# Kernel optimization log

Hardware: AMD Instinct MI355X
Metric: run time of the kernel (lower is better)

## Reference

```python
import jax, jax.numpy as jnp
import numpy as np

N = 1_000_000      # total atoms
B = 1024           # number of molecules (batch segments)
NUM_ELEMENTS = 118
D_EMB = 64
D_HID = 128


def setup_inputs() -> dict:
    key = jax.random.key(0)
    ks = jax.random.split(key, 9)
    positions = jax.random.normal(ks[0], (N, 3), dtype=jnp.float32) * 5.0
    atomic_numbers = jax.random.randint(ks[1], (N,), 0, NUM_ELEMENTS, dtype=jnp.int64)
    batch = jnp.sort(jax.random.randint(ks[2], (N,), 0, B, dtype=jnp.int64))
    # learned parameters (torch Linear is y = x @ W.T + b; we store W as (in, out))
    embed = jax.random.normal(ks[3], (NUM_ELEMENTS, D_EMB), dtype=jnp.float32) * 0.1
    W1 = jax.random.normal(ks[4], (D_EMB, D_HID), dtype=jnp.float32) * (1.0 / np.sqrt(D_EMB))
    b1 = jnp.zeros((D_HID,), dtype=jnp.float32)
    W2 = jax.random.normal(ks[5], (D_HID, D_HID), dtype=jnp.float32) * (1.0 / np.sqrt(D_HID))
    b2 = jnp.zeros((D_HID,), dtype=jnp.float32)
    W3 = jax.random.normal(ks[6], (D_HID, 1), dtype=jnp.float32) * (1.0 / np.sqrt(D_HID))
    b3 = jnp.zeros((1,), dtype=jnp.float32)
    return {
        "positions": positions,
        "embed": embed,
        "W1": W1, "b1": b1,
        "W2": W2, "b2": b2,
        "W3": W3, "b3": b3,
        "atomic_numbers": atomic_numbers,
        "batch": batch,
    }


def reference(positions, embed, W1, b1, W2, b2, W3, b3, atomic_numbers, batch):
    def energy_fn(pos):
        h = embed[atomic_numbers]                       # [N, 64] gather
        pos_feat = jnp.sum(pos, axis=-1, keepdims=True) # [N, 1]
        h = h + 0.0 * pos_feat                          # keeps pos in the graph (grad is zero)
        x = jax.nn.silu(h @ W1 + b1)                    # [N, 128]
        x = jax.nn.silu(x @ W2 + b2)                    # [N, 128]
        per_atom = (x @ W3 + b3)[:, 0]                  # [N]
        # energy.scatter_add_(0, batch, per_atom)
        return jax.ops.segment_sum(per_atom, batch, num_segments=B)  # [B]

    energy = energy_fn(positions)
    # forces = -grad_R sum(V(R)); identically zero here but computed faithfully
    forces = -jax.grad(lambda p: energy_fn(p).sum())(positions)      # [N, 3]
    return (energy, forces)
```

## Files before the change

kernel.cpp:

```cpp
#include <hip/hip_runtime.h>

#define D_EMB   64
#define D_HID   128
#define NUM_EL  118
#define CHUNK   1024
#define NBINS   16

__global__ __launch_bounds__(256)
void mace_etab_kernel(const float* __restrict__ embed,
                      const float* __restrict__ W1, const float* __restrict__ b1,
                      const float* __restrict__ W2, const float* __restrict__ b2,
                      const float* __restrict__ W3, const float* __restrict__ b3,
                      float* __restrict__ Etab, float* __restrict__ energy, int B) {
    __shared__ float h[D_EMB];
    __shared__ float x1[D_HID];
    __shared__ float part[D_HID];
    __shared__ float wsum[2];
    const int t  = threadIdx.x;
    const int j  = t & 127;
    const int hf = t >> 7;
    const int zz = blockIdx.x;

    for (int i = blockIdx.x * 256 + t; i < B; i += NUM_EL * 256)
        energy[i] = 0.f;

    if (t < D_EMB) h[t] = embed[zz * D_EMB + t];
    __syncthreads();

    {
        const int k0 = hf * 32;
        float a0 = 0.f, a1 = 0.f, a2 = 0.f, a3 = 0.f;
        #pragma unroll
        for (int k = 0; k < 32; k += 4) {
            a0 = fmaf(h[k0 + k + 0], W1[(k0 + k + 0) * D_HID + j], a0);
            a1 = fmaf(h[k0 + k + 1], W1[(k0 + k + 1) * D_HID + j], a1);
            a2 = fmaf(h[k0 + k + 2], W1[(k0 + k + 2) * D_HID + j], a2);
            a3 = fmaf(h[k0 + k + 3], W1[(k0 + k + 3) * D_HID + j], a3);
        }
        const float p = (a0 + a1) + (a2 + a3);
        if (hf == 1) part[j] = p;
        __syncthreads();
        if (hf == 0) {
            const float acc = b1[j] + p + part[j];
            x1[j] = acc / (1.0f + expf(-acc));
        }
        __syncthreads();
    }

    {
        const int k0 = hf * 64;
        float a0 = 0.f, a1 = 0.f, a2 = 0.f, a3 = 0.f;
        #pragma unroll
        for (int k = 0; k < 64; k += 4) {
            a0 = fmaf(x1[k0 + k + 0], W2[(k0 + k + 0) * D_HID + j], a0);
            a1 = fmaf(x1[k0 + k + 1], W2[(k0 + k + 1) * D_HID + j], a1);
            a2 = fmaf(x1[k0 + k + 2], W2[(k0 + k + 2) * D_HID + j], a2);
            a3 = fmaf(x1[k0 + k + 3], W2[(k0 + k + 3) * D_HID + j], a3);
        }
        const float p = (a0 + a1) + (a2 + a3);
        if (hf == 1) part[j] = p;
        __syncthreads();

        float r = 0.f;
        if (hf == 0) {
            const float acc2 = b2[j] + p + part[j];
            const float s2 = acc2 / (1.0f + expf(-acc2));
            r = s2 * W3[j];
        }
        #pragma unroll
        for (int off = 32; off > 0; off >>= 1)
            r += __shfl_down(r, off, 64);
        if (hf == 0 && (t & 63) == 0) wsum[t >> 6] = r;
        __syncthreads();
        if (t == 0) Etab[zz] = wsum[0] + wsum[1] + b3[0];
    }
}

__global__ __launch_bounds__(256)
void mace_sum_kernel(const int* __restrict__ z,
                     const int* __restrict__ batch,
                     const float* __restrict__ EtabG,
                     float* __restrict__ energy,
                     float4* __restrict__ forces4,
                     int n, int nblk, int nf4) {
    __shared__ float etab_s[NUM_EL];
    __shared__ float bins[NBINS];
    __shared__ int   base_s;
    const int t   = threadIdx.x;
    const int bid = blockIdx.x;
    const int chunk = bid * CHUNK;

    if (t < NUM_EL) etab_s[t] = EtabG[t];
    if (t < NBINS)  bins[t] = 0.f;
    if (t == 0)     base_s = batch[chunk];

    for (int i = bid * 256 + t; i < nf4; i += nblk * 256)
        forces4[i] = make_float4(0.f, 0.f, 0.f, 0.f);

    __syncthreads();
    const int base = base_s;

    const int i4 = (chunk >> 2) + t;
    if (i4 < (n >> 2)) {
        const int4 zv = ((const int4*)z)[i4];
        const int4 bv = ((const int4*)batch)[i4];
        const float e0 = etab_s[zv.x], e1 = etab_s[zv.y];
        const float e2 = etab_s[zv.z], e3 = etab_s[zv.w];

        float acc = e0;
        int   bc  = bv.x;
        #define FLUSH()                                                     \
            do {                                                            \
                const int bin = bc - base;                                  \
                if (bin < NBINS) atomicAdd(&bins[bin], acc);                \
                else             atomicAdd(&energy[bc], acc);               \
            } while (0)
        if (bv.y == bc) acc += e1; else { FLUSH(); bc = bv.y; acc = e1; }
        if (bv.z == bc) acc += e2; else { FLUSH(); bc = bv.z; acc = e2; }
        if (bv.w == bc) acc += e3; else { FLUSH(); bc = bv.w; acc = e3; }
        FLUSH();
        #undef FLUSH
    }

    if (bid == nblk - 1 && t == 0) {
        for (int i = (n >> 2) << 2; i < n; ++i)
            atomicAdd(&energy[batch[i]], etab_s[z[i]]);
    }

    __syncthreads();
    if (t < NBINS) {
        const float v = bins[t];
        if (v != 0.f) atomicAdd(&energy[base + t], v);
    }
}

extern "C" void kernel_launch(void* const* d_in, const int* in_sizes, int n_in,
                              void* d_out, int out_size, void* d_ws, size_t ws_size,
                              hipStream_t stream) {
    const float* embed = (const float*)d_in[1];
    const float* W1    = (const float*)d_in[2];
    const float* b1    = (const float*)d_in[3];
    const float* W2    = (const float*)d_in[4];
    const float* b2    = (const float*)d_in[5];
    const float* W3    = (const float*)d_in[6];
    const float* b3    = (const float*)d_in[7];
    const int*   z     = (const int*)d_in[8];
    const int*   batch = (const int*)d_in[9];
    const int    n     = in_sizes[8];

    const int B    = out_size - 3 * n;
    const int nf4  = (3 * n) / 4;
    const int nblk = (n + CHUNK - 1) / CHUNK;

    float*  energy  = (float*)d_out;
    float4* forces4 = (float4*)((float*)d_out + B);
    float*  Etab    = (float*)d_ws;

    mace_etab_kernel<<<NUM_EL, 256, 0, stream>>>(embed, W1, b1, W2, b2, W3, b3,
                                                 Etab, energy, B);
    mace_sum_kernel<<<nblk, 256, 0, stream>>>(z, batch, Etab, energy, forces4,
                                              n, nblk, nf4);
}
```

Before: 15.25 us.

## Replace atomic segment sum with per-chunk element histograms and per-molecule reduction

The first kernel now zeroes forces and builds, for each 1024-atom chunk, a histogram of atomic numbers per molecule slot, plus the segment start offsets. It also computes the per-element energy table in extra blocks of the same launch. A second kernel, one block per molecule, turns the histogram counts and the table into a dot product, falling back to direct gathers for slots beyond the histogram, and writes energy directly without global atomics. This removes the global float atomics and makes the sum deterministic, at the cost of a larger histogram write and read and serial boundary loops for empty molecules.

```diff
diff --git a/kernel.cpp b/kernel.cpp
--- a/kernel.cpp
+++ b/kernel.cpp
@@ -3,69 +3,131 @@
 #define D_EMB   64
 #define D_HID   128
 #define NUM_EL  118
+#define HPAD    120
+#define NSLOT   4
 #define CHUNK   1024
-#define NBINS   16
+#define K1_GRID 2048
 
 __global__ __launch_bounds__(256)
-void mace_etab_kernel(const float* __restrict__ embed,
+void mace_prep_kernel(const float* __restrict__ embed,
                       const float* __restrict__ W1, const float* __restrict__ b1,
                       const float* __restrict__ W2, const float* __restrict__ b2,
                       const float* __restrict__ W3, const float* __restrict__ b3,
-                      float* __restrict__ Etab, float* __restrict__ energy, int B) {
-    __shared__ float h[D_EMB];
-    __shared__ float x1[D_HID];
-    __shared__ float part[D_HID];
-    __shared__ float wsum[2];
-    const int t  = threadIdx.x;
-    const int j  = t & 127;
-    const int hf = t >> 7;
-    const int zz = blockIdx.x;
-
-    for (int i = blockIdx.x * 256 + t; i < B; i += NUM_EL * 256)
-        energy[i] = 0.f;
-
-    if (t < D_EMB) h[t] = embed[zz * D_EMB + t];
-    __syncthreads();
+                      const int* __restrict__ z,
+                      const int* __restrict__ batch,
+                      float* __restrict__ Etab,
+                      int* __restrict__ starts,
+                      int* __restrict__ chunkbase,
+                      int* __restrict__ hist,
+                      float4* __restrict__ forces4,
+                      int nf4, int n, int B, int nchunk) {
+    const int t   = threadIdx.x;
+    const int bid = blockIdx.x;
 
     {
-        const int k0 = hf * 32;
-        float a0 = 0.f, a1 = 0.f, a2 = 0.f, a3 = 0.f;
-        #pragma unroll
-        for (int k = 0; k < 32; k += 4) {
-            a0 = fmaf(h[k0 + k + 0], W1[(k0 + k + 0) * D_HID + j], a0);
-            a1 = fmaf(h[k0 + k + 1], W1[(k0 + k + 1) * D_HID + j], a1);
-            a2 = fmaf(h[k0 + k + 2], W1[(k0 + k + 2) * D_HID + j], a2);
-            a3 = fmaf(h[k0 + k + 3], W1[(k0 + k + 3) * D_HID + j], a3);
-        }
-        const float p = (a0 + a1) + (a2 + a3);
-        if (hf == 1) part[j] = p;
-        __syncthreads();
-        if (hf == 0) {
-            const float acc = b1[j] + p + part[j];
-            x1[j] = acc / (1.0f + expf(-acc));
-        }
-        __syncthreads();
+        const float4 z4f = make_float4(0.f, 0.f, 0.f, 0.f);
+        for (int i = bid * 256 + t; i < nf4; i += K1_GRID * 256)
+            forces4[i] = z4f;
     }
 
-    {
-        const int k0 = hf * 64;
-        float a0 = 0.f, a1 = 0.f, a2 = 0.f, a3 = 0.f;
-        #pragma unroll
-        for (int k = 0; k < 64; k += 4) {
-            a0 = fmaf(x1[k0 + k + 0], W2[(k0 + k + 0) * D_HID + j], a0);
-            a1 = fmaf(x1[k0 + k + 1], W2[(k0 + k + 1) * D_HID + j], a1);
-            a2 = fmaf(x1[k0 + k + 2], W2[(k0 + k + 2) * D_HID + j], a2);
-            a3 = fmaf(x1[k0 + k + 3], W2[(k0 + k + 3) * D_HID + j], a3);
-        }
-        const float p = (a0 + a1) + (a2 + a3);
-        if (hf == 1) part[j] = p;
-        __syncthreads();
-
+    if (bid < nchunk) {
+        __shared__ unsigned int shist[NSLOT * HPAD];
+        __shared__ int base_s;
+
+        for (int i = t; i < NSLOT * HPAD; i += 256) shist[i] = 0u;
+
+        const int n4 = n >> 2;
+        const int i4 = (bid << 8) + t;
+        const bool valid = (i4 < n4);
+        int4 zv = make_int4(0,0,0,0), bv = make_int4(0,0,0,0);
+        if (valid) {
+            zv = ((const int4*)z)[i4];
+            bv = ((const int4*)batch)[i4];
+        }
+        if (t == 0) base_s = bv.x;
+        __syncthreads();
+        const int base = base_s;
+
+        if (valid) {
+            const int s0 = bv.x - base, s1 = bv.y - base;
+            const int s2 = bv.z - base, s3 = bv.w - base;
+            if (s0 < NSLOT) atomicAdd(&shist[s0 * HPAD + zv.x], 1u);
+            if (s1 < NSLOT) atomicAdd(&shist[s1 * HPAD + zv.y], 1u);
+            if (s2 < NSLOT) atomicAdd(&shist[s2 * HPAD + zv.z], 1u);
+            if (s3 < NSLOT) atomicAdd(&shist[s3 * HPAD + zv.w], 1u);
+
+            const int idx = i4 << 2;
+            if (bv.x != bv.y) { for (int b = bv.x + 1; b <= bv.y; ++b) starts[b] = idx + 1; }
+            if (bv.y != bv.z) { for (int b = bv.y + 1; b <= bv.z; ++b) starts[b] = idx + 2; }
+            if (bv.z != bv.w) { for (int b = bv.z + 1; b <= bv.w; ++b) starts[b] = idx + 3; }
+            if (idx + 4 < n) {
+                const int nx = batch[idx + 4];
+                if (bv.w != nx) { for (int b = bv.w + 1; b <= nx; ++b) starts[b] = idx + 4; }
+            }
+        }
+        if (t == 0) {
+            chunkbase[bid] = base;
+            if (bid == 0) {
+                const int first = batch[0], last = batch[n - 1];
+                for (int b = 0; b <= first; ++b) starts[b] = 0;
+                for (int b = last + 1; b <= B; ++b) starts[b] = n;
+            }
+        }
+        __syncthreads();
+
+        int* __restrict__ hrow = hist + (size_t)bid * (NSLOT * HPAD);
+        for (int i = t; i < NSLOT * HPAD; i += 256) hrow[i] = (int)shist[i];
+
+    } else if (bid < nchunk + NUM_EL) {
+        __shared__ float h[D_EMB];
+        __shared__ float x1[D_HID];
+        __shared__ float part[D_HID];
+        __shared__ float wsum[2];
+        const int zz = bid - nchunk;
+        const int j  = t & 127;
+        const int hf = t >> 7;
+
+        if (t < D_EMB) h[t] = embed[zz * D_EMB + t];
+        __syncthreads();
+
+        {
+            const int k0 = hf * 32;
+            float a0 = 0.f, a1 = 0.f, a2 = 0.f, a3 = 0.f;
+            #pragma unroll
+            for (int k = 0; k < 32; k += 4) {
+                a0 = fmaf(h[k0 + k + 0], W1[(k0 + k + 0) * D_HID + j], a0);
+                a1 = fmaf(h[k0 + k + 1], W1[(k0 + k + 1) * D_HID + j], a1);
+                a2 = fmaf(h[k0 + k + 2], W1[(k0 + k + 2) * D_HID + j], a2);
+                a3 = fmaf(h[k0 + k + 3], W1[(k0 + k + 3) * D_HID + j], a3);
+            }
+            const float p = (a0 + a1) + (a2 + a3);
+            if (hf == 1) part[j] = p;
+            __syncthreads();
+            if (hf == 0) {
+                const float acc = b1[j] + p + part[j];
+                x1[j] = acc / (1.0f + expf(-acc));
+            }
+            __syncthreads();
+        }
         float r = 0.f;
-        if (hf == 0) {
-            const float acc2 = b2[j] + p + part[j];
-            const float s2 = acc2 / (1.0f + expf(-acc2));
-            r = s2 * W3[j];
+        {
+            const int k0 = hf * 64;
+            float a0 = 0.f, a1 = 0.f, a2 = 0.f, a3 = 0.f;
+            #pragma unroll
+            for (int k = 0; k < 64; k += 4) {
+                a0 = fmaf(x1[k0 + k + 0], W2[(k0 + k + 0) * D_HID + j], a0);
+                a1 = fmaf(x1[k0 + k + 1], W2[(k0 + k + 1) * D_HID + j], a1);
+                a2 = fmaf(x1[k0 + k + 2], W2[(k0 + k + 2) * D_HID + j], a2);
+                a3 = fmaf(x1[k0 + k + 3], W2[(k0 + k + 3) * D_HID + j], a3);
+            }
+            const float p = (a0 + a1) + (a2 + a3);
+            if (hf == 1) part[j] = p;
+            __syncthreads();
+            if (hf == 0) {
+                const float acc2 = b2[j] + p + part[j];
+                const float s2 = acc2 / (1.0f + expf(-acc2));
+                r = s2 * W3[j];
+            }
         }
         #pragma unroll
         for (int off = 32; off > 0; off >>= 1)
@@ -77,61 +139,48 @@
 }
 
 __global__ __launch_bounds__(256)
-void mace_sum_kernel(const int* __restrict__ z,
-                     const int* __restrict__ batch,
-                     const float* __restrict__ EtabG,
-                     float* __restrict__ energy,
-                     float4* __restrict__ forces4,
-                     int n, int nblk, int nf4) {
+void mace_energy_kernel(const int* __restrict__ z,
+                        const int* __restrict__ starts,
+                        const int* __restrict__ chunkbase,
+                        const int* __restrict__ hist,
+                        const float* __restrict__ EtabG,
+                        float* __restrict__ energy, int n) {
     __shared__ float etab_s[NUM_EL];
-    __shared__ float bins[NBINS];
-    __shared__ int   base_s;
-    const int t   = threadIdx.x;
-    const int bid = blockIdx.x;
-    const int chunk = bid * CHUNK;
+    __shared__ float wsum[4];
+    const int b = blockIdx.x;
+    const int t = threadIdx.x;
 
     if (t < NUM_EL) etab_s[t] = EtabG[t];
-    if (t < NBINS)  bins[t] = 0.f;
-    if (t == 0)     base_s = batch[chunk];
-
-    for (int i = bid * 256 + t; i < nf4; i += nblk * 256)
-        forces4[i] = make_float4(0.f, 0.f, 0.f, 0.f);
-
+    const int start = starts[b];
+    const int end   = starts[b + 1];
     __syncthreads();
-    const int base = base_s;
-
-    const int i4 = (chunk >> 2) + t;
-    if (i4 < (n >> 2)) {
-        const int4 zv = ((const int4*)z)[i4];
-        const int4 bv = ((const int4*)batch)[i4];
-        const float e0 = etab_s[zv.x], e1 = etab_s[zv.y];
-        const float e2 = etab_s[zv.z], e3 = etab_s[zv.w];
-
-        float acc = e0;
-        int   bc  = bv.x;
-        #define FLUSH()                                                     \
-            do {                                                            \
-                const int bin = bc - base;                                  \
-                if (bin < NBINS) atomicAdd(&bins[bin], acc);                \
-                else             atomicAdd(&energy[bc], acc);               \
-            } while (0)
-        if (bv.y == bc) acc += e1; else { FLUSH(); bc = bv.y; acc = e1; }
-        if (bv.z == bc) acc += e2; else { FLUSH(); bc = bv.z; acc = e2; }
-        if (bv.w == bc) acc += e3; else { FLUSH(); bc = bv.w; acc = e3; }
-        FLUSH();
-        #undef FLUSH
+
+    float acc = 0.f;
+    if (end > start) {
+        const int c0 = start >> 10;
+        const int c1 = (end - 1) >> 10;
+        for (int c = c0; c <= c1; ++c) {
+            const int slot = b - chunkbase[c];
+            if (slot < NSLOT) {
+                if (t < NUM_EL) {
+                    const int cnt = hist[((size_t)c * NSLOT + slot) * HPAD + t];
+                    acc = fmaf((float)cnt, etab_s[t], acc);
+                }
+            } else {
+                const int lo = max(start, c << 10);
+                const int hi = min(end, (c + 1) << 10);
+                for (int i = lo + t; i < hi; i += 256)
+                    acc += etab_s[z[i]];
+            }
+        }
     }
 
-    if (bid == nblk - 1 && t == 0) {
-        for (int i = (n >> 2) << 2; i < n; ++i)
-            atomicAdd(&energy[batch[i]], etab_s[z[i]]);
-    }
-
+    #pragma unroll
+    for (int off = 32; off > 0; off >>= 1)
+        acc += __shfl_down(acc, off, 64);
+    if ((t & 63) == 0) wsum[t >> 6] = acc;
     __syncthreads();
-    if (t < NBINS) {
-        const float v = bins[t];
-        if (v != 0.f) atomicAdd(&energy[base + t], v);
-    }
+    if (t == 0) energy[b] = (wsum[0] + wsum[1]) + (wsum[2] + wsum[3]);
 }
 
 extern "C" void kernel_launch(void* const* d_in, const int* in_sizes, int n_in,
@@ -144,20 +193,27 @@
     const float* b2    = (const float*)d_in[5];
     const float* W3    = (const float*)d_in[6];
     const float* b3    = (const float*)d_in[7];
-    const int*   z     = (const int*)d_in[8];
+    const int*   zp    = (const int*)d_in[8];
     const int*   batch = (const int*)d_in[9];
     const int    n     = in_sizes[8];
 
-    const int B    = out_size - 3 * n;
-    const int nf4  = (3 * n) / 4;
-    const int nblk = (n + CHUNK - 1) / CHUNK;
+    const int B      = out_size - 3 * n;
+    const int nf4    = (3 * n) / 4;
+    const int nchunk = (n + CHUNK - 1) / CHUNK;
 
     float*  energy  = (float*)d_out;
     float4* forces4 = (float4*)((float*)d_out + B);
-    float*  Etab    = (float*)d_ws;
-
-    mace_etab_kernel<<<NUM_EL, 256, 0, stream>>>(embed, W1, b1, W2, b2, W3, b3,
-                                                 Etab, energy, B);
-    mace_sum_kernel<<<nblk, 256, 0, stream>>>(z, batch, Etab, energy, forces4,
-                                              n, nblk, nf4);
+
+    char* ws = (char*)d_ws;
+    float* Etab      = (float*)(ws);
+    int*   starts    = (int*)(ws + 512);
+    int*   chunkbase = (int*)(ws + 8192);
+    int*   hist      = (int*)(ws + 16384);
+
+    mace_prep_kernel<<<K1_GRID, 256, 0, stream>>>(embed, W1, b1, W2, b2, W3, b3,
+                                                  zp, batch, Etab, starts,
+                                                  chunkbase, hist, forces4,
+                                                  nf4, n, B, nchunk);
+    mace_energy_kernel<<<B, 256, 0, stream>>>(zp, starts, chunkbase, hist,
+                                              Etab, energy, n);
 }
```

Result: faster. 13.91 us (-8.8%).
